# Performance work log

Measured on AMD Instinct MI355X. Metric: run time of the kernel, lower is better.

The kernel has to match this reference:

```python
import jax, jax.numpy as jnp
import numpy as np

N_ITEMS = 200000
EMB = 100
LAYERS = 3
N_EDGES = 6400000


def setup_inputs() -> dict:
    key = jax.random.key(0)
    k1, k2, k3, k4, k5 = jax.random.split(key, 5)
    embedding = jax.random.normal(k1, (N_ITEMS, EMB), dtype=jnp.float32)
    adj_vals = jax.random.uniform(k2, (N_EDGES,), dtype=jnp.float32)
    weights = jax.random.normal(k3, (LAYERS, EMB, EMB), dtype=jnp.float32) * (1.0 / np.sqrt(EMB))
    adj_rows = jax.random.randint(k4, (N_EDGES,), 0, N_ITEMS, dtype=jnp.int32)
    adj_cols = jax.random.randint(k5, (N_EDGES,), 0, N_ITEMS, dtype=jnp.int32)
    return {"embedding": embedding, "adj_vals": adj_vals, "weights": weights,
            "adj_rows": adj_rows, "adj_cols": adj_cols}


def reference(embedding, adj_vals, weights, adj_rows, adj_cols):
    # embedding: [N, d]; weights: [L, d, d] (torch Linear weight, y = x @ W.T)
    # adjacency in COO: out[r] += v * x[c]
    n = embedding.shape[0]
    eps = 1e-12  # F.normalize eps
    x = embedding
    finals = [x]  # layer-0 copy is NOT normalized (matches original)
    for i in range(weights.shape[0]):
        x = jnp.einsum('nd,ed->ne', x, weights[i])          # linear, no bias
        gathered = adj_vals[:, None] * x[adj_cols]           # [E, d]
        x = jax.ops.segment_sum(gathered, adj_rows, num_segments=n)  # SpMM
        norm = jnp.maximum(jnp.linalg.norm(x, axis=-1, keepdims=True), eps)
        finals.append(x / norm)  # appended copy normalized; carried x stays raw
    return jnp.mean(jnp.stack(finals, axis=0), axis=0)
```

## Files before the change

### kernel.cpp

```cpp
#include <hip/hip_runtime.h>

#define EMB 100
#define XSTRIDE 52
#define Y8DW 32
#define BSHIFT 8
#define BROWS 256
#define MAXBUCK 1024
#define CAP 9216
#define CHUNK 4096
#define EPT (CHUNK / 256)

typedef __attribute__((ext_vector_type(8))) short short8;
typedef __attribute__((ext_vector_type(4))) float f32x4;
typedef __attribute__((ext_vector_type(2))) float f2v;

__device__ __forceinline__ unsigned packbf(float a, float b) {
    unsigned ua = __float_as_uint(a), ub = __float_as_uint(b);
    unsigned ra = (ua + 0x7FFFu + ((ua >> 16) & 1u)) >> 16;
    unsigned rb = (ub + 0x7FFFu + ((ub >> 16) & 1u)) >> 16;
    return ra | (rb << 16);
}

__device__ __forceinline__ unsigned char f32_to_fp8(float f) {
    unsigned u = __float_as_uint(f);
    unsigned s = (u >> 24) & 0x80u;
    unsigned mag = u & 0x7FFFFFFFu;
    if (mag >= 0x43E00000u) return (unsigned char)(s | 0x7Eu);
    if (mag < 0x3C800000u) {
        int r = __float2int_rn(__uint_as_float(mag) * 512.f);
        return (unsigned char)(s | (unsigned)r);
    }
    unsigned r = mag + 0x7FFFFu + ((mag >> 20) & 1u);
    unsigned e = r >> 23, m = (r >> 20) & 7u;
    return (unsigned char)(s | ((e - 120u) << 3) | m);
}

__device__ __forceinline__ unsigned pack4_fp8(float a0, float a1, float a2, float a3) {
#if __has_builtin(__builtin_amdgcn_cvt_pk_fp8_f32)
    int lo = __builtin_amdgcn_cvt_pk_fp8_f32(a0, a1, 0, false);
    return (unsigned)__builtin_amdgcn_cvt_pk_fp8_f32(a2, a3, lo, true);
#else
    return (unsigned)f32_to_fp8(a0) | ((unsigned)f32_to_fp8(a1) << 8) |
           ((unsigned)f32_to_fp8(a2) << 16) | ((unsigned)f32_to_fp8(a3) << 24);
#endif
}

__device__ __forceinline__ void fma_fp8x4(unsigned g, float v,
                                          float& a0, float& a1, float& a2, float& a3) {
#if __has_builtin(__builtin_amdgcn_cvt_pk_f32_fp8)
    f2v lo = __builtin_amdgcn_cvt_pk_f32_fp8((int)g, false);
    f2v hi = __builtin_amdgcn_cvt_pk_f32_fp8((int)g, true);
    a0 = fmaf(v, lo[0], a0); a1 = fmaf(v, lo[1], a1);
    a2 = fmaf(v, hi[0], a2); a3 = fmaf(v, hi[1], a3);
#else
    float o[4];
#pragma unroll
    for (int d = 0; d < 4; ++d) {
        unsigned b = (g >> (8 * d)) & 0xFFu;
        unsigned e = (b >> 3) & 15u, m = b & 7u;
        float val = e ? __uint_as_float(((e + 120u) << 23) | (m << 20))
                      : (float)m * (1.f / 512.f);
        o[d] = (b & 0x80u) ? -val : val;
    }
    a0 = fmaf(v, o[0], a0); a1 = fmaf(v, o[1], a1);
    a2 = fmaf(v, o[2], a2); a3 = fmaf(v, o[3], a3);
#endif
}

__global__ __launch_bounds__(256) void k_partition(const int* __restrict__ rows,
                                                   const int* __restrict__ cols,
                                                   const float* __restrict__ vals,
                                                   int* __restrict__ bucket_cnt,
                                                   int2* __restrict__ part,
                                                   int E, int nbuck) {
    __shared__ int hist[MAXBUCK];
    __shared__ int loc[MAXBUCK];
    __shared__ int base_s[MAXBUCK];
    __shared__ int scan256[256];
    __shared__ int2 stage[CHUNK];
    int tid = threadIdx.x;
    int base = blockIdx.x * CHUNK;
    int nE = E - base; if (nE > CHUNK) nE = CHUNK;

    for (int s = tid; s < nbuck; s += 256) hist[s] = 0;
    __syncthreads();

    int r_[EPT]; unsigned cv_[EPT]; int rk_[EPT];
#pragma unroll
    for (int k = 0; k < EPT; ++k) {
        int o = tid + k * 256;
        if (o < nE) {
            int i = base + o;
            int r = rows[i];
            unsigned q = (unsigned)__float2int_rn(vals[i] * 16383.f);
            r_[k] = r;
            cv_[k] = (unsigned)cols[i] | (q << 18);
            rk_[k] = atomicAdd(&hist[r >> BSHIFT], 1);
        } else r_[k] = -1;
    }
    __syncthreads();

    for (int s = tid; s < nbuck; s += 256)
        base_s[s] = hist[s] ? atomicAdd(&bucket_cnt[s], hist[s]) : 0;

    int s4 = tid * 4;
    int h0 = (s4     < nbuck) ? hist[s4]     : 0;
    int h1 = (s4 + 1 < nbuck) ? hist[s4 + 1] : 0;
    int h2 = (s4 + 2 < nbuck) ? hist[s4 + 2] : 0;
    int h3 = (s4 + 3 < nbuck) ? hist[s4 + 3] : 0;
    int tot = h0 + h1 + h2 + h3;
    scan256[tid] = tot;
    __syncthreads();
    for (int off = 1; off < 256; off <<= 1) {
        int t = (tid >= off) ? scan256[tid - off] : 0;
        __syncthreads();
        scan256[tid] += t;
        __syncthreads();
    }
    int excl = scan256[tid] - tot;
    if (s4     < nbuck) loc[s4]     = excl;
    if (s4 + 1 < nbuck) loc[s4 + 1] = excl + h0;
    if (s4 + 2 < nbuck) loc[s4 + 2] = excl + h0 + h1;
    if (s4 + 3 < nbuck) loc[s4 + 3] = excl + h0 + h1 + h2;
    __syncthreads();

#pragma unroll
    for (int k = 0; k < EPT; ++k) {
        if (r_[k] >= 0) {
            int b = r_[k] >> BSHIFT;
            stage[loc[b] + rk_[k]] = make_int2(r_[k], (int)cv_[k]);
        }
    }
    __syncthreads();

    for (int k = tid; k < nE; k += 256) {
        int2 e = stage[k];
        int b = e.x >> BSHIFT;
        int pos = base_s[b] + (k - loc[b]);
        if (pos < CAP)
            part[(size_t)b * CAP + pos] = e;
    }
}

__global__ __launch_bounds__(1024) void k_scan2(const int* __restrict__ cnt,
                                                int* __restrict__ basearr, int nb) {
    __shared__ int tmp[1024];
    int v = (threadIdx.x < nb) ? cnt[threadIdx.x] : 0;
    tmp[threadIdx.x] = v;
    __syncthreads();
    for (int off = 1; off < 1024; off <<= 1) {
        int t = (threadIdx.x >= off) ? tmp[threadIdx.x - off] : 0;
        __syncthreads();
        tmp[threadIdx.x] += t;
        __syncthreads();
    }
    if (threadIdx.x < nb) basearr[threadIdx.x] = tmp[threadIdx.x] - v;
}

__global__ __launch_bounds__(256) void k_build_csr(const int2* __restrict__ part,
                                                   const int* __restrict__ bucket_cnt,
                                                   const int* __restrict__ bucket_base,
                                                   int* __restrict__ row_ptr,
                                                   unsigned* __restrict__ csr,
                                                   int N, int E) {
    __shared__ int cnt[BROWS];
    __shared__ int scn[BROWS];
    __shared__ int cur[BROWS];
    int b = blockIdx.x;
    int tid = threadIdx.x;
    int cntb = bucket_cnt[b];
    const int2* seg = part + (size_t)b * CAP;
    int cbase = bucket_base[b];
    int rowbase = b << BSHIFT;

    cnt[tid] = 0;
    __syncthreads();
    for (int i = tid; i < cntb; i += 256)
        atomicAdd(&cnt[seg[i].x - rowbase], 1);
    __syncthreads();
    int v = cnt[tid];
    scn[tid] = v;
    __syncthreads();
    for (int off = 1; off < 256; off <<= 1) {
        int t = (tid >= off) ? scn[tid - off] : 0;
        __syncthreads();
        scn[tid] += t;
        __syncthreads();
    }
    int rp = cbase + scn[tid] - v;
    if (rowbase + tid < N) row_ptr[rowbase + tid] = rp;
    cur[tid] = rp;
    if (b == 0 && tid == 0) row_ptr[N] = E;
    __syncthreads();
    for (int i = tid; i < cntb; i += 256) {
        int2 e = seg[i];
        int pos = atomicAdd(&cur[e.x - rowbase], 1);
        csr[pos] = (unsigned)e.y;
    }
}

template <bool F32SRC>
__global__ __launch_bounds__(256) void k_gemm_mfma(const void* __restrict__ Xv,
                                                   const float* __restrict__ W,
                                                   unsigned* __restrict__ Y8,
                                                   int nTiles, int N) {
    __shared__ uint4 Bf[28][64];
    int tid = threadIdx.x;
#pragma unroll
    for (int it = 0; it < 7; ++it) {
        int id = it * 256 + tid;
        int fs = id >> 6, lane = id & 63;
        int nt = fs >> 2, ks = fs & 3;
        int e = nt * 16 + (lane & 15);
        int dbase = ks * 32 + (lane >> 4) * 8;
        float w[8];
#pragma unroll
        for (int j = 0; j < 8; ++j) {
            int d = dbase + j;
            w[j] = (e < EMB && d < EMB) ? W[e * EMB + d] : 0.f;
        }
        uint4 u;
        u.x = packbf(w[0], w[1]); u.y = packbf(w[2], w[3]);
        u.z = packbf(w[4], w[5]); u.w = packbf(w[6], w[7]);
        Bf[fs][lane] = u;
    }
    __syncthreads();

    int wid = (blockIdx.x * 256 + tid) >> 6;
    int nWaves = gridDim.x * 4;
    int lane = tid & 63;
    int m = lane & 15, kg = lane >> 4;

    for (int tile = wid; tile < nTiles; tile += nWaves) {
        int rowbase = tile * 16;
        int arow = rowbase + m; if (arow >= N) arow = N - 1;
        uint4 a[4];
        if (F32SRC) {
            const float* xr = (const float*)Xv + (size_t)arow * EMB;
#pragma unroll
            for (int ks = 0; ks < 3; ++ks) {
                float4 v0 = *(const float4*)(xr + ks * 32 + kg * 8);
                float4 v1 = *(const float4*)(xr + ks * 32 + kg * 8 + 4);
                a[ks] = make_uint4(packbf(v0.x, v0.y), packbf(v0.z, v0.w),
                                   packbf(v1.x, v1.y), packbf(v1.z, v1.w));
            }
            uint4 t = make_uint4(0, 0, 0, 0);
            if (kg == 0) { float4 v = *(const float4*)(xr + 96);
                           t.x = packbf(v.x, v.y); t.y = packbf(v.z, v.w); }
            a[3] = t;
        } else {
            const unsigned* xr = (const unsigned*)Xv + (size_t)arow * XSTRIDE;
#pragma unroll
            for (int ks = 0; ks < 3; ++ks)
                a[ks] = *(const uint4*)(xr + ks * 16 + kg * 4);
            uint4 t = make_uint4(0, 0, 0, 0);
            if (kg == 0) { uint2 v = *(const uint2*)(xr + 48); t.x = v.x; t.y = v.y; }
            a[3] = t;
        }

        f32x4 acc[7];
#pragma unroll
        for (int nt = 0; nt < 7; ++nt) acc[nt] = (f32x4){0.f, 0.f, 0.f, 0.f};
#pragma unroll
        for (int ks = 0; ks < 4; ++ks) {
            short8 av = __builtin_bit_cast(short8, a[ks]);
#pragma unroll
            for (int nt = 0; nt < 7; ++nt) {
                short8 bv = __builtin_bit_cast(short8, Bf[nt * 4 + ks][lane]);
                acc[nt] = __builtin_amdgcn_mfma_f32_16x16x32_bf16(bv, av, acc[nt], 0, 0, 0);
            }
        }
        int rr = rowbase + m;
        if (rr < N) {
            unsigned* yrow = Y8 + ((size_t)rr << 5) + kg;
#pragma unroll
            for (int nt = 0; nt < 6; ++nt)
                yrow[nt * 4] = pack4_fp8(acc[nt][0], acc[nt][1], acc[nt][2], acc[nt][3]);
            if (kg == 0)
                yrow[24] = pack4_fp8(acc[6][0], acc[6][1], acc[6][2], acc[6][3]);
            else
                yrow[24] = 0;
            yrow[28] = 0;
        }
    }
}

__global__ __launch_bounds__(256) void k_spmm_norm(const int* __restrict__ row_ptr,
                                                   const unsigned* __restrict__ csr,
                                                   const unsigned* __restrict__ Y8,
                                                   unsigned* __restrict__ Xout,
                                                   float* __restrict__ Out,
                                                   const float* __restrict__ prev,
                                                   float pscale, float scale,
                                                   int writeX, int N) {
    int wave = (blockIdx.x * 256 + threadIdx.x) >> 6;
    int lane = threadIdx.x & 63;
    if (wave >= N) return;
    int g = lane >> 3, lg = lane & 7;
    int beg = row_ptr[wave], end = row_ptr[wave + 1];
    const float dq = 1.0f / 16383.f;
    float a[16];
#pragma unroll
    for (int k = 0; k < 16; ++k) a[k] = 0.f;
    const uint4* Yb = (const uint4*)((const char*)Y8 + lg * 16);

    for (int j0 = beg; j0 < end; j0 += 32) {
#pragma unroll
        for (int t = 0; t < 4; ++t) {
            int je = j0 + t * 8 + g;
            bool ok = je < end;
            unsigned u = __builtin_nontemporal_load(&csr[ok ? je : beg]);
            float v = ok ? (float)(u >> 18) : 0.f;
            uint4 gg = Yb[(size_t)(u & 0x3FFFFu) << 3];
            fma_fp8x4(gg.x, v, a[0], a[1], a[2], a[3]);
            fma_fp8x4(gg.y, v, a[4], a[5], a[6], a[7]);
            fma_fp8x4(gg.z, v, a[8], a[9], a[10], a[11]);
            fma_fp8x4(gg.w, v, a[12], a[13], a[14], a[15]);
        }
    }

#pragma unroll
    for (int k = 0; k < 16; ++k) {
        float t = a[k];
        t += __shfl_xor(t, 8, 64);
        t += __shfl_xor(t, 16, 64);
        t += __shfl_xor(t, 32, 64);
        a[k] = t;
    }
    float ss = 0.f;
#pragma unroll
    for (int k = 0; k < 16; ++k) ss = fmaf(a[k], a[k], ss);
    ss += __shfl_xor(ss, 1, 64);
    ss += __shfl_xor(ss, 2, 64);
    ss += __shfl_xor(ss, 4, 64);
    float so = scale / fmaxf(sqrtf(ss), 1e-8f);

    if (lane < 32) {
        int dbase = lg * 16 + g * 4;
        if (dbase < EMB) {
            float w0 = a[g * 4 + 0], w1 = a[g * 4 + 1];
            float w2 = a[g * 4 + 2], w3 = a[g * 4 + 3];
            if (writeX) {
                uint2 xw;
                xw.x = packbf(w0 * dq, w1 * dq);
                xw.y = packbf(w2 * dq, w3 * dq);
                *(uint2*)(Xout + (size_t)wave * XSTRIDE + (dbase >> 1)) = xw;
            }
            float4 p = *(const float4*)(prev + (size_t)wave * EMB + dbase);
            float4 o;
            o.x = fmaf(w0, so, p.x * pscale);
            o.y = fmaf(w1, so, p.y * pscale);
            o.z = fmaf(w2, so, p.z * pscale);
            o.w = fmaf(w3, so, p.w * pscale);
            *(float4*)(Out + (size_t)wave * EMB + dbase) = o;
        }
    }
}

extern "C" void kernel_launch(void* const* d_in, const int* in_sizes, int n_in,
                              void* d_out, int out_size, void* d_ws, size_t ws_size,
                              hipStream_t stream) {
    const float* emb   = (const float*)d_in[0];
    const float* avals = (const float*)d_in[1];
    const float* wts   = (const float*)d_in[2];
    const int*   arows = (const int*)d_in[3];
    const int*   acols = (const int*)d_in[4];

    const int N = in_sizes[0] / EMB;
    const int E = in_sizes[1];
    const int L = in_sizes[2] / (EMB * EMB);
    const float scale = 1.0f / (float)(L + 1);
    const int nbuck = (N + BROWS - 1) >> BSHIFT;

    unsigned* Y8      = (unsigned*)d_ws;
    unsigned* bufX    = Y8 + (size_t)N * Y8DW;
    int* row_ptr      = (int*)(bufX + (size_t)N * XSTRIDE);
    int* bucket_cnt   = row_ptr + (N + 2);
    int* bucket_base  = bucket_cnt + MAXBUCK;
    unsigned* csr     = (unsigned*)(bucket_base + MAXBUCK);
    int2* part        = (int2*)d_ws;
    float* out = (float*)d_out;

    const int nchunk = (E + CHUNK - 1) / CHUNK;

    hipMemsetAsync(bucket_cnt, 0, MAXBUCK * sizeof(int), stream);
    k_partition<<<nchunk, 256, 0, stream>>>(arows, acols, avals, bucket_cnt,
                                            part, E, nbuck);
    k_scan2<<<1, 1024, 0, stream>>>(bucket_cnt, bucket_base, nbuck);
    k_build_csr<<<nbuck, 256, 0, stream>>>(part, bucket_cnt, bucket_base,
                                           row_ptr, csr, N, E);

    const int nTiles = (N + 15) / 16;
    const int gemm_blocks = 782;
    const int spmm_blocks = (N + 3) / 4;

    k_gemm_mfma<true><<<gemm_blocks, 256, 0, stream>>>(emb, wts, Y8, nTiles, N);
    k_spmm_norm<<<spmm_blocks, 256, 0, stream>>>(row_ptr, csr, Y8, bufX,
                                                 out, emb, scale, scale, 1, N);
    for (int l = 1; l < L; ++l) {
        k_gemm_mfma<false><<<gemm_blocks, 256, 0, stream>>>(
            bufX, wts + (size_t)l * EMB * EMB, Y8, nTiles, N);
        k_spmm_norm<<<spmm_blocks, 256, 0, stream>>>(row_ptr, csr, Y8, bufX,
                                                     out, out, 1.0f, scale,
                                                     (l < L - 1) ? 1 : 0, N);
    }
}
```

Measured before the change: 851.5 us.

## Restructure SpMM gather to per-lane dword loads with two edge streams per wave

Rewrites the SpMM kernel so each wave splits into two halves that process alternating edges, with 25 lanes each loading one 4-byte fp8 chunk per neighbor instead of 8-lane groups loading 16-byte chunks. Edge loops are unrolled by 8 and 4 with loads batched ahead of the FMAs to raise memory-level parallelism, and the cross-lane reduction shrinks to one shuffle per accumulator. The value dequant scale moves into the gather, and the producer no longer writes zero padding into the Y8 rows. The trade is many more narrow gather transactions per edge in exchange for less reduction work and more loads in flight.

```diff
diff --git a/kernel.cpp b/kernel.cpp
--- a/kernel.cpp
+++ b/kernel.cpp
@@ -278,9 +278,6 @@
                 yrow[nt * 4] = pack4_fp8(acc[nt][0], acc[nt][1], acc[nt][2], acc[nt][3]);
             if (kg == 0)
                 yrow[24] = pack4_fp8(acc[6][0], acc[6][1], acc[6][2], acc[6][3]);
-            else
-                yrow[24] = 0;
-            yrow[28] = 0;
         }
     }
 }
@@ -296,64 +293,66 @@
     int wave = (blockIdx.x * 256 + threadIdx.x) >> 6;
     int lane = threadIdx.x & 63;
     if (wave >= N) return;
-    int g = lane >> 3, lg = lane & 7;
+    int half = lane >> 5, sub = lane & 31;
     int beg = row_ptr[wave], end = row_ptr[wave + 1];
     const float dq = 1.0f / 16383.f;
-    float a[16];
-#pragma unroll
-    for (int k = 0; k < 16; ++k) a[k] = 0.f;
-    const uint4* Yb = (const uint4*)((const char*)Y8 + lg * 16);
-
-    for (int j0 = beg; j0 < end; j0 += 32) {
-#pragma unroll
-        for (int t = 0; t < 4; ++t) {
-            int je = j0 + t * 8 + g;
-            bool ok = je < end;
-            unsigned u = __builtin_nontemporal_load(&csr[ok ? je : beg]);
-            float v = ok ? (float)(u >> 18) : 0.f;
-            uint4 gg = Yb[(size_t)(u & 0x3FFFFu) << 3];
-            fma_fp8x4(gg.x, v, a[0], a[1], a[2], a[3]);
-            fma_fp8x4(gg.y, v, a[4], a[5], a[6], a[7]);
-            fma_fp8x4(gg.z, v, a[8], a[9], a[10], a[11]);
-            fma_fp8x4(gg.w, v, a[12], a[13], a[14], a[15]);
-        }
-    }
-
-#pragma unroll
-    for (int k = 0; k < 16; ++k) {
-        float t = a[k];
-        t += __shfl_xor(t, 8, 64);
-        t += __shfl_xor(t, 16, 64);
-        t += __shfl_xor(t, 32, 64);
-        a[k] = t;
-    }
-    float ss = 0.f;
-#pragma unroll
-    for (int k = 0; k < 16; ++k) ss = fmaf(a[k], a[k], ss);
-    ss += __shfl_xor(ss, 1, 64);
-    ss += __shfl_xor(ss, 2, 64);
-    ss += __shfl_xor(ss, 4, 64);
-    float so = scale / fmaxf(sqrtf(ss), 1e-8f);
-
-    if (lane < 32) {
-        int dbase = lg * 16 + g * 4;
-        if (dbase < EMB) {
-            float w0 = a[g * 4 + 0], w1 = a[g * 4 + 1];
-            float w2 = a[g * 4 + 2], w3 = a[g * 4 + 3];
-            if (writeX) {
-                uint2 xw;
-                xw.x = packbf(w0 * dq, w1 * dq);
-                xw.y = packbf(w2 * dq, w3 * dq);
-                *(uint2*)(Xout + (size_t)wave * XSTRIDE + (dbase >> 1)) = xw;
-            }
-            float4 p = *(const float4*)(prev + (size_t)wave * EMB + dbase);
-            float4 o;
-            o.x = fmaf(w0, so, p.x * pscale);
-            o.y = fmaf(w1, so, p.y * pscale);
-            o.z = fmaf(w2, so, p.z * pscale);
-            o.w = fmaf(w3, so, p.w * pscale);
-            *(float4*)(Out + (size_t)wave * EMB + dbase) = o;
-        }
+    float a0 = 0.f, a1 = 0.f, a2 = 0.f, a3 = 0.f;
+    if (sub < 25) {
+        const unsigned* yb = Y8 + sub;
+        int j = beg + half;
+        for (; j + 14 < end; j += 16) {
+            unsigned u[8], g[8];
+#pragma unroll
+            for (int t = 0; t < 8; ++t)
+                u[t] = __builtin_nontemporal_load(&csr[j + 2 * t]);
+#pragma unroll
+            for (int t = 0; t < 8; ++t)
+                g[t] = yb[(u[t] & 0x3FFFFu) << 5];
+#pragma unroll
+            for (int t = 0; t < 8; ++t)
+                fma_fp8x4(g[t], (float)(u[t] >> 18) * dq, a0, a1, a2, a3);
+        }
+        for (; j + 6 < end; j += 8) {
+            unsigned u[4], g[4];
+#pragma unroll
+            for (int t = 0; t < 4; ++t)
+                u[t] = __builtin_nontemporal_load(&csr[j + 2 * t]);
+#pragma unroll
+            for (int t = 0; t < 4; ++t)
+                g[t] = yb[(u[t] & 0x3FFFFu) << 5];
+#pragma unroll
+            for (int t = 0; t < 4; ++t)
+                fma_fp8x4(g[t], (float)(u[t] >> 18) * dq, a0, a1, a2, a3);
+        }
+        for (; j < end; j += 2) {
+            unsigned u = csr[j];
+            unsigned g = yb[(u & 0x3FFFFu) << 5];
+            float v = (float)(u >> 18) * dq;
+            fma_fp8x4(g, v, a0, a1, a2, a3);
+        }
+    }
+    a0 += __shfl_xor(a0, 32, 64);
+    a1 += __shfl_xor(a1, 32, 64);
+    a2 += __shfl_xor(a2, 32, 64);
+    a3 += __shfl_xor(a3, 32, 64);
+    float ss = fmaf(a0, a0, fmaf(a1, a1, fmaf(a2, a2, a3 * a3)));
+#pragma unroll
+    for (int off = 16; off; off >>= 1) ss += __shfl_xor(ss, off, 64);
+    float sc = scale / fmaxf(sqrtf(ss), 1e-12f);
+    if (half == 0 && sub < 25) {
+        if (writeX) {
+            uint2 xw;
+            xw.x = packbf(a0, a1); xw.y = packbf(a2, a3);
+            *(uint2*)(Xout + (size_t)wave * XSTRIDE + sub * 2) = xw;
+        }
+        const float4* pp = (const float4*)(prev + (size_t)wave * EMB) + sub;
+        float4 p = *pp;
+        float4 o;
+        o.x = fmaf(a0, sc, p.x * pscale);
+        o.y = fmaf(a1, sc, p.y * pscale);
+        o.z = fmaf(a2, sc, p.z * pscale);
+        o.w = fmaf(a3, sc, p.w * pscale);
+        *((float4*)(Out + (size_t)wave * EMB) + sub) = o;
     }
 }
 
```

Measured after the change: 785.8 us. -7.7%, faster.
